# Optimization experiments

Hardware: AMD Instinct MI355X
Metric: run time of the kernel (lower is better)

Reference implementation:

```python
import jax, jax.numpy as jnp
import numpy as np

EPS = 1e-5  # InstanceNorm2d default eps


def setup_inputs() -> dict:
    key = jax.random.key(0)
    k1, k2, k3, k4, k5, k6 = jax.random.split(key, 6)
    B, N, C, KV, H = 8, 4096, 512, 960, 4
    dq, dk = C // 4, KV // 4
    emb1 = jax.random.normal(k1, (B, N, C), dtype=jnp.float32)
    emb_all = jax.random.normal(k2, (B, N, KV), dtype=jnp.float32)
    # per-head query Linear weights (torch Linear weight is [out, in]); 4 distinct heads
    Wq = jax.random.normal(k3, (H, dq, dq), dtype=jnp.float32) * 0.05
    # key/value: the original forward only ever uses key[0] / value[0]
    Wk = jax.random.normal(k4, (dk, dk), dtype=jnp.float32) * 0.05
    Wv = jax.random.normal(k5, (dk, dk), dtype=jnp.float32) * 0.05
    Wo = jax.random.normal(k6, (C, C), dtype=jnp.float32) * 0.05
    return {"emb1": emb1, "emb_all": emb_all, "Wq": Wq, "Wk": Wk, "Wv": Wv, "Wo": Wo}


def reference(emb1, emb_all, Wq, Wk, Wv, Wo):
    B, N, C = emb1.shape
    KV = emb_all.shape[2]
    dq, dk = C // 4, KV // 4
    # split emb1 into 4 chunks along channels -> [B, N, 4, dq], apply per-head query Linear
    Qc = emb1.reshape(B, N, 4, dq)
    Q = jnp.einsum("bnhd,hed->bhne", Qc, Wq)            # [B,4,N,dq]
    # all 4 K and V chunks use key[0]/value[0] (as in the source)
    Kc = emb_all.reshape(B, N, 4, dk)
    K = jnp.einsum("bnhd,ed->bhne", Kc, Wk)             # [B,4,N,dk]
    V = jnp.einsum("bnhd,ed->bhne", Kc, Wv)             # [B,4,N,dk]
    # channel attention: contract over tokens N -> scores [B,4,dq,dk]
    scores = jnp.einsum("bhnc,bhnk->bhck", Q, K) / jnp.sqrt(jnp.float32(KV))
    # InstanceNorm2d (no affine): normalize each (b, head) score map over (dq, dk)
    mu = scores.mean(axis=(2, 3), keepdims=True)
    var = scores.var(axis=(2, 3), keepdims=True)        # biased variance, matches torch
    normed = (scores - mu) * jax.lax.rsqrt(var + EPS)
    probs = jax.nn.softmax(normed, axis=3)              # softmax over dk
    # dropout is identity in eval mode
    context = jnp.einsum("bhck,bhnk->bhcn", probs, V)   # [B,4,dq,N]
    # permute(0,3,2,1) -> [B,N,dq,4], flatten last two -> [B,N,C]
    context = jnp.transpose(context, (0, 3, 2, 1)).reshape(B, N, C)
    O1 = jnp.einsum("bnc,ec->bne", context, Wo)         # out Linear, no bias
    return O1
```

## Files before the change

kernel.cpp:

```cpp
#include <hip/hip_runtime.h>
#include <cstdint>
#include <cstddef>

#define B_ 8
#define N_ 4096
#define C_ 512
#define KV_ 960
#define DQ 128
#define DK 240
#define NSPLIT 16

typedef __attribute__((ext_vector_type(8))) short bf16x8;
typedef __attribute__((ext_vector_type(4))) float f32x4;
#define AS1 __attribute__((address_space(1)))
#define AS3 __attribute__((address_space(3)))

__device__ __forceinline__ ushort f2bf(float f) {
  uint32_t u = __float_as_uint(f);
  u += 0x7FFFu + ((u >> 16) & 1u);
  return (ushort)(u >> 16);
}

__device__ __forceinline__ uint32_t cvtpk(float lo, float hi) {
  uint32_t r;
  asm("v_cvt_pk_bf16_f32 %0, %1, %2" : "=v"(r) : "v"(lo), "v"(hi));
  return r;
}

union bfpack {
  uint32_t u[4];
  ushort s[8];
  bf16x8 v;
};

__global__ __launch_bounds__(512) void k1_mfma(const float* __restrict__ emb1,
                                               const ushort* __restrict__ embaBF,
                                               float* __restrict__ P) {
  __shared__ ushort As[128 * 64];
  __shared__ ushort Bs[128 * 64];
  const int bh = blockIdx.x;
  const int split = blockIdx.y;
  const int jh = blockIdx.z;
  const int b = bh >> 2, h = bh & 3;
  const int t = threadIdx.x;
  const int w = t >> 6, l = t & 63;
  const int wm = w >> 1, wn = w & 1;

  const float* Abase = emb1 + (size_t)b * N_ * C_ + h * DQ;
  const ushort* Bbase = embaBF + (size_t)b * N_ * KV_;

  const int cA = t & 127;
  const int jB = t & 127;
  const int nb0 = t >> 7;
  int jl = jh * 128 + jB;
  if (jl > DK - 1) jl = DK - 1;
  const int jg = h * DK + jl;

  f32x4 acc[2][4];
#pragma unroll
  for (int fm = 0; fm < 2; ++fm)
#pragma unroll
    for (int fn = 0; fn < 4; ++fn) acc[fm][fn] = (f32x4){0.f, 0.f, 0.f, 0.f};

  const int n0 = split * (N_ / NSPLIT);
  const int lrow = l & 15;
  const int KS = (N_ / NSPLIT) / 64;

  float va[2][8];
  ushort ub[2][8];

#pragma unroll
  for (int q = 0; q < 2; ++q) {
    const float* g = Abase + (size_t)(n0 + (nb0 + q * 4) * 8) * C_ + cA;
#pragma unroll
    for (int kk = 0; kk < 8; ++kk) va[q][kk] = g[(size_t)kk * C_];
  }
#pragma unroll
  for (int q = 0; q < 2; ++q) {
    const ushort* g = Bbase + (size_t)(n0 + (nb0 + q * 4) * 8) * KV_ + jg;
#pragma unroll
    for (int kk = 0; kk < 8; ++kk) ub[q][kk] = g[(size_t)kk * KV_];
  }

  for (int ks = 0; ks < KS; ++ks) {
    bfpack pa[2], pb[2];
#pragma unroll
    for (int q = 0; q < 2; ++q)
#pragma unroll
      for (int p = 0; p < 4; ++p) pa[q].u[p] = cvtpk(va[q][2 * p], va[q][2 * p + 1]);
#pragma unroll
    for (int q = 0; q < 2; ++q)
#pragma unroll
      for (int kk = 0; kk < 8; ++kk) pb[q].s[kk] = ub[q][kk];

    __builtin_amdgcn_s_barrier();

#pragma unroll
    for (int q = 0; q < 2; ++q) {
      const int nb = nb0 + q * 4;
      *(bf16x8*)(As + cA * 64 + ((nb ^ (cA & 7)) << 3)) = pa[q].v;
      *(bf16x8*)(Bs + jB * 64 + ((nb ^ (jB & 7)) << 3)) = pb[q].v;
    }

    if (ks + 1 < KS) {
      const int nb1 = n0 + (ks + 1) * 64;
#pragma unroll
      for (int q = 0; q < 2; ++q) {
        const float* g = Abase + (size_t)(nb1 + (nb0 + q * 4) * 8) * C_ + cA;
#pragma unroll
        for (int kk = 0; kk < 8; ++kk) va[q][kk] = g[(size_t)kk * C_];
      }
#pragma unroll
      for (int q = 0; q < 2; ++q) {
        const ushort* g = Bbase + (size_t)(nb1 + (nb0 + q * 4) * 8) * KV_ + jg;
#pragma unroll
        for (int kk = 0; kk < 8; ++kk) ub[q][kk] = g[(size_t)kk * KV_];
      }
    }

    asm volatile("s_waitcnt lgkmcnt(0)" ::: "memory");
    __builtin_amdgcn_sched_barrier(0);
    __builtin_amdgcn_s_barrier();

#pragma unroll
    for (int half = 0; half < 2; ++half) {
      const int kb = half * 4 + (l >> 4);
      bf16x8 af[2], bv[4];
#pragma unroll
      for (int fm = 0; fm < 2; ++fm) {
        const int i = wm * 32 + fm * 16 + lrow;
        af[fm] = *(const bf16x8*)(As + i * 64 + ((kb ^ (i & 7)) << 3));
      }
#pragma unroll
      for (int fn = 0; fn < 4; ++fn) {
        const int j = wn * 64 + fn * 16 + lrow;
        bv[fn] = *(const bf16x8*)(Bs + j * 64 + ((kb ^ (j & 7)) << 3));
      }
#pragma unroll
      for (int fm = 0; fm < 2; ++fm)
#pragma unroll
        for (int fn = 0; fn < 4; ++fn)
          acc[fm][fn] = __builtin_amdgcn_mfma_f32_16x16x32_bf16(af[fm], bv[fn],
                                                                acc[fm][fn], 0, 0, 0);
    }
  }
  f32x4* Pv4 = (f32x4*)P + ((size_t)(split * 32 + bh) * 2 + jh) * 4096;
#pragma unroll
  for (int fm = 0; fm < 2; ++fm)
#pragma unroll
    for (int fn = 0; fn < 4; ++fn) Pv4[(fm * 4 + fn) * 512 + t] = acc[fm][fn];
}

__global__ __launch_bounds__(256) void k_reduce_frag(const f32x4* __restrict__ P,
                                                     float* __restrict__ S) {
  const int bh = blockIdx.x;
  const int g = blockIdx.y * 256 + threadIdx.x;
  const int jh = g >> 12;
  const int rest = g & 4095;
  f32x4 a = P[((size_t)bh * 2 + jh) * 4096 + rest];
#pragma unroll
  for (int s = 1; s < NSPLIT; ++s) {
    f32x4 v = P[((size_t)(s * 32 + bh) * 2 + jh) * 4096 + rest];
    a.x += v.x; a.y += v.y; a.z += v.z; a.w += v.w;
  }
  const int v = rest >> 9, tt = rest & 511;
  const int fm = v >> 2, fn = v & 3;
  const int wv = tt >> 6, l = tt & 63;
  const int wm = wv >> 1, wn = wv & 1;
  const int i0 = wm * 32 + fm * 16 + (l >> 4) * 4;
  const int j = jh * 128 + wn * 64 + fn * 16 + (l & 15);
  if (j < DK) {
    float* sp = S + (size_t)bh * (DQ * DK) + (size_t)i0 * DK + j;
    sp[0] = a.x; sp[DK] = a.y; sp[2 * DK] = a.z; sp[3 * DK] = a.w;
  }
}

__global__ __launch_bounds__(256) void k_cvt(const float4* __restrict__ in,
                                             ushort4* __restrict__ out, int n4) {
  int i = blockIdx.x * 256 + threadIdx.x;
  if (i >= n4) return;
  float4 v = in[i];
  ushort4 o;
  o.x = f2bf(v.x); o.y = f2bf(v.y); o.z = f2bf(v.z); o.w = f2bf(v.w);
  out[i] = o;
}

__global__ __launch_bounds__(256) void k_g1(const float* __restrict__ Wq,
                                            const float* __restrict__ S,
                                            float* __restrict__ U) {
  const int h = blockIdx.x, c0 = blockIdx.y * 64;
  const int b = blockIdx.z / 5, n0 = (blockIdx.z % 5) * 48;
  const float* A = Wq + (size_t)h * 16384;
  const float* Bp = S + (size_t)(b * 4 + h) * 30720 + n0;
  float* Cp = U + (size_t)(b * 4 + h) * 30720 + n0;
  __shared__ float Ast[16][65];
  __shared__ float Bst[16][49];
  const int t = threadIdx.x;
  const int mi = (t >> 4) * 4, nj = (t & 15) * 3;
  float acc[4][3] = {};
  for (int k0 = 0; k0 < 128; k0 += 16) {
    __syncthreads();
#pragma unroll
    for (int q = 0; q < 4; ++q) {
      int idx = t + q * 256, m = idx >> 4, k = idx & 15;
      Ast[k][m] = A[(size_t)(c0 + m) * 128 + k0 + k];
    }
#pragma unroll
    for (int q = 0; q < 3; ++q) {
      int idx = t + q * 256, k = idx / 48, n = idx % 48;
      Bst[k][n] = Bp[(size_t)(k0 + k) * 240 + n];
    }
    __syncthreads();
#pragma unroll
    for (int kk = 0; kk < 16; ++kk) {
      float a4[4], b3[3];
#pragma unroll
      for (int x = 0; x < 4; ++x) a4[x] = Ast[kk][mi + x];
#pragma unroll
      for (int y = 0; y < 3; ++y) b3[y] = Bst[kk][nj + y];
#pragma unroll
      for (int x = 0; x < 4; ++x)
#pragma unroll
        for (int y = 0; y < 3; ++y) acc[x][y] = fmaf(a4[x], b3[y], acc[x][y]);
    }
  }
#pragma unroll
  for (int x = 0; x < 4; ++x)
#pragma unroll
    for (int y = 0; y < 3; ++y)
      Cp[(size_t)(c0 + mi + x) * 240 + nj + y] = acc[x][y];
}

__global__ __launch_bounds__(256) void k_g2(const float* __restrict__ U,
                                            const float* __restrict__ Wk,
                                            float* __restrict__ SC) {
  const int m0 = blockIdx.x * 64, n0 = blockIdx.y * 48;
  __shared__ float Ast[16][65];
  __shared__ float Bst2[48][17];
  const int t = threadIdx.x;
  const int mi = (t >> 4) * 4, nj = (t & 15) * 3;
  float acc[4][3] = {};
  for (int k0 = 0; k0 < 240; k0 += 16) {
    __syncthreads();
#pragma unroll
    for (int q = 0; q < 4; ++q) {
      int idx = t + q * 256, m = idx >> 4, k = idx & 15;
      Ast[k][m] = U[(size_t)(m0 + m) * 240 + k0 + k];
    }
#pragma unroll
    for (int q = 0; q < 3; ++q) {
      int idx = t + q * 256, n = idx >> 4, kd = idx & 15;
      Bst2[n][kd] = Wk[(size_t)(n0 + n) * 240 + k0 + kd];
    }
    __syncthreads();
#pragma unroll
    for (int kk = 0; kk < 16; ++kk) {
      float a4[4], b3[3];
#pragma unroll
      for (int x = 0; x < 4; ++x) a4[x] = Ast[kk][mi + x];
#pragma unroll
      for (int y = 0; y < 3; ++y) b3[y] = Bst2[nj + y][kk];
#pragma unroll
      for (int x = 0; x < 4; ++x)
#pragma unroll
        for (int y = 0; y < 3; ++y) acc[x][y] = fmaf(a4[x], b3[y], acc[x][y]);
    }
  }
  const float scale = 0.0322748612183951f;
#pragma unroll
  for (int x = 0; x < 4; ++x)
#pragma unroll
    for (int y = 0; y < 3; ++y)
      SC[(size_t)(m0 + mi + x) * 240 + n0 + nj + y] = acc[x][y] * scale;
}

__global__ __launch_bounds__(256) void k_g3(const float* __restrict__ PR,
                                            const float* __restrict__ Wv,
                                            float* __restrict__ T) {
  const int m0 = blockIdx.x * 64, n0 = blockIdx.y * 48;
  __shared__ float Ast[16][65];
  __shared__ float Bst[16][49];
  const int t = threadIdx.x;
  const int mi = (t >> 4) * 4, nj = (t & 15) * 3;
  float acc[4][3] = {};
  for (int k0 = 0; k0 < 240; k0 += 16) {
    __syncthreads();
#pragma unroll
    for (int q = 0; q < 4; ++q) {
      int idx = t + q * 256, m = idx >> 4, k = idx & 15;
      Ast[k][m] = PR[(size_t)(m0 + m) * 240 + k0 + k];
    }
#pragma unroll
    for (int q = 0; q < 3; ++q) {
      int idx = t + q * 256, k = idx / 48, n = idx % 48;
      Bst[k][n] = Wv[(size_t)(k0 + k) * 240 + n0 + n];
    }
    __syncthreads();
#pragma unroll
    for (int kk = 0; kk < 16; ++kk) {
      float a4[4], b3[3];
#pragma unroll
      for (int x = 0; x < 4; ++x) a4[x] = Ast[kk][mi + x];
#pragma unroll
      for (int y = 0; y < 3; ++y) b3[y] = Bst[kk][nj + y];
#pragma unroll
      for (int x = 0; x < 4; ++x)
#pragma unroll
        for (int y = 0; y < 3; ++y) acc[x][y] = fmaf(a4[x], b3[y], acc[x][y]);
    }
  }
#pragma unroll
  for (int x = 0; x < 4; ++x)
#pragma unroll
    for (int y = 0; y < 3; ++y)
      T[(size_t)(m0 + mi + x) * 240 + n0 + nj + y] = acc[x][y];
}

__global__ __launch_bounds__(256) void k_g4(const float* __restrict__ Wo,
                                            const float* __restrict__ T,
                                            ushort* __restrict__ W3bf) {
  const int h = blockIdx.x, e0 = blockIdx.y * 64;
  const int b = blockIdx.z / 5, n0 = (blockIdx.z % 5) * 48;
  const float* Bp = T + (size_t)(b * 4 + h) * 30720 + n0;
  ushort* Cp = W3bf + (size_t)b * 491520 + h * 240 + n0;
  __shared__ float Ast[16][65];
  __shared__ float Bst[16][49];
  const int t = threadIdx.x;
  const int mi = (t >> 4) * 4, nj = (t & 15) * 3;
  float acc[4][3] = {};
  for (int k0 = 0; k0 < 128; k0 += 16) {
    __syncthreads();
#pragma unroll
    for (int q = 0; q < 4; ++q) {
      int idx = t + q * 256, m = idx >> 4, k = idx & 15;
      Ast[k][m] = Wo[(size_t)(e0 + m) * 512 + 4 * (k0 + k) + h];
    }
#pragma unroll
    for (int q = 0; q < 3; ++q) {
      int idx = t + q * 256, k = idx / 48, n = idx % 48;
      Bst[k][n] = Bp[(size_t)(k0 + k) * 240 + n];
    }
    __syncthreads();
#pragma unroll
    for (int kk = 0; kk < 16; ++kk) {
      float a4[4], b3[3];
#pragma unroll
      for (int x = 0; x < 4; ++x) a4[x] = Ast[kk][mi + x];
#pragma unroll
      for (int y = 0; y < 3; ++y) b3[y] = Bst[kk][nj + y];
#pragma unroll
      for (int x = 0; x < 4; ++x)
#pragma unroll
        for (int y = 0; y < 3; ++y) acc[x][y] = fmaf(a4[x], b3[y], acc[x][y]);
    }
  }
#pragma unroll
  for (int x = 0; x < 4; ++x)
#pragma unroll
    for (int y = 0; y < 3; ++y)
      Cp[(size_t)(e0 + mi + x) * 960 + nj + y] = f2bf(acc[x][y]);
}

__global__ __launch_bounds__(1024) void k_stats(const float* __restrict__ SC,
                                                float* __restrict__ stats) {
  const int bh = blockIdx.x;
  const float* s = SC + (size_t)bh * 30720;
  const int t = threadIdx.x;
  float sum = 0.f, sq = 0.f;
  for (int i = t; i < 30720; i += 1024) {
    float v = s[i];
    sum += v;
    sq = fmaf(v, v, sq);
  }
#pragma unroll
  for (int o = 32; o > 0; o >>= 1) {
    sum += __shfl_down(sum, o);
    sq += __shfl_down(sq, o);
  }
  __shared__ float s1[16], s2[16];
  if ((t & 63) == 0) { s1[t >> 6] = sum; s2[t >> 6] = sq; }
  __syncthreads();
  if (t == 0) {
    float ts = 0.f, tq = 0.f;
#pragma unroll
    for (int i = 0; i < 16; ++i) { ts += s1[i]; tq += s2[i]; }
    const float mu = ts * (1.f / 30720.f);
    const float var = tq * (1.f / 30720.f) - mu * mu;
    stats[bh * 2] = mu;
    stats[bh * 2 + 1] = rsqrtf(var + 1e-5f);
  }
}

__global__ __launch_bounds__(512) void k_softmax(const float* __restrict__ SC,
                                                 const float* __restrict__ stats,
                                                 float* __restrict__ PR) {
  const int bh = blockIdx.x;
  const float mu = stats[bh * 2], rstd = stats[bh * 2 + 1];
  const int wv = threadIdx.x >> 6, l = threadIdx.x & 63;
  const int row0 = blockIdx.y * 32 + wv * 4;
  const float* s = SC + (size_t)bh * 30720;
  float* p = PR + (size_t)bh * 30720;
#pragma unroll
  for (int r = 0; r < 4; ++r) {
    const float* srow = s + (size_t)(row0 + r) * 240;
    float* prow = p + (size_t)(row0 + r) * 240;
    float x0 = (srow[l] - mu) * rstd;
    float x1 = (srow[64 + l] - mu) * rstd;
    float x2 = (srow[128 + l] - mu) * rstd;
    float x3 = (l < 48) ? (srow[192 + l] - mu) * rstd : -1e30f;
    float m = fmaxf(fmaxf(x0, x1), fmaxf(x2, x3));
#pragma unroll
    for (int o = 32; o > 0; o >>= 1) m = fmaxf(m, __shfl_xor(m, o));
    float e0 = __expf(x0 - m), e1 = __expf(x1 - m), e2 = __expf(x2 - m);
    float e3 = (l < 48) ? __expf(x3 - m) : 0.f;
    float ss = e0 + e1 + e2 + e3;
#pragma unroll
    for (int o = 32; o > 0; o >>= 1) ss += __shfl_xor(ss, o);
    const float inv = 1.f / ss;
    prow[l] = e0 * inv;
    prow[64 + l] = e1 * inv;
    prow[128 + l] = e2 * inv;
    if (l < 48) prow[192 + l] = e3 * inv;
  }
}

__global__ __launch_bounds__(512) void k3_mfma(const ushort* __restrict__ A,
                                               const ushort* __restrict__ Bw,
                                               float* __restrict__ C) {
  __shared__ ushort LDSu[3][16384];
  const int bid = blockIdx.x;
  const int swz = (bid & 7) * 32 + (bid >> 3);
  const int b = swz >> 5;
  const int rem = swz & 31;
  const int mt = rem >> 1, nt = rem & 1;
  const int t = threadIdx.x;
  const int w = t >> 6, l = t & 63;
  const int wr = w >> 2, wc = w & 3;

  const ushort* Ab = A + (size_t)b * N_ * KV_ + (size_t)mt * 256 * KV_;
  const ushort* Bb = Bw + (size_t)b * C_ * KV_ + (size_t)nt * 256 * KV_;

  const int r_l = l & 15;
  const int c_l = (l >> 4) * 8;

#define K3STAGE(k0, bf)                                                        \
  do {                                                                         \
    _Pragma("unroll") for (int inst = 0; inst < 2; ++inst) {                   \
      const int g = w * 2 + inst;                             \
      const ushort* ga = Ab + (size_t)(g * 16 + r_l) * KV_ + (k0) + c_l;       \
      __builtin_amdgcn_global_load_lds(                                        \
          (AS1 const uint32_t*)(uintptr_t)ga,                                  \
          (AS3 uint32_t*)(uintptr_t)(&LDSu[bf][0] + g * 512), 16, 0, 0);       \
      const ushort* gb = Bb + (size_t)(g * 16 + r_l) * KV_ + (k0) + c_l;       \
      __builtin_amdgcn_global_load_lds(                                        \
          (AS1 const uint32_t*)(uintptr_t)gb,                                  \
          (AS3 uint32_t*)(uintptr_t)(&LDSu[bf][8192] + g * 512), 16, 0, 0);    \
    }                                                                          \
  } while (0)

  f32x4 acc[8][4];
#pragma unroll
  for (int fm = 0; fm < 8; ++fm)
#pragma unroll
    for (int fn = 0; fn < 4; ++fn) acc[fm][fn] = (f32x4){0.f, 0.f, 0.f, 0.f};

  K3STAGE(0, 0);
  K3STAGE(32, 1);

  const int NK = KV_ / 32;
  int cbuf = 0, sbuf = 2;
  for (int ks = 0; ks < NK; ++ks) {
    if (ks < NK - 1) asm volatile("s_waitcnt vmcnt(4)" ::: "memory");
    else             asm volatile("s_waitcnt vmcnt(0)" ::: "memory");
    __builtin_amdgcn_sched_barrier(0);
    __builtin_amdgcn_s_barrier();
    if (ks + 2 < NK) K3STAGE((ks + 2) * 32, sbuf);
    const ushort* Abase = &LDSu[cbuf][0];
    const ushort* Bbase = &LDSu[cbuf][8192];
    bf16x8 af[8], bv[4];
#pragma unroll
    for (int f = 0; f < 8; ++f)
      af[f] = *(const bf16x8*)(Abase + (wr * 8 + f) * 512 + l * 8);
#pragma unroll
    for (int f = 0; f < 4; ++f)
      bv[f] = *(const bf16x8*)(Bbase + (wc * 4 + f) * 512 + l * 8);
#pragma unroll
    for (int fm = 0; fm < 8; ++fm)
#pragma unroll
      for (int fn = 0; fn < 4; ++fn)
        acc[fm][fn] = __builtin_amdgcn_mfma_f32_16x16x32_bf16(af[fm], bv[fn],
                                                              acc[fm][fn], 0, 0, 0);
    cbuf = (cbuf == 2) ? 0 : cbuf + 1;
    sbuf = (sbuf == 2) ? 0 : sbuf + 1;
  }
#undef K3STAGE

  float* Cb = C + (size_t)b * N_ * C_ + ((size_t)mt * 256) * C_ + nt * 256;
  const int col = wc * 64 + (l & 15);
  const int rbase = wr * 128 + (l >> 4) * 4;
#pragma unroll
  for (int fm = 0; fm < 8; ++fm)
#pragma unroll
    for (int fn = 0; fn < 4; ++fn)
#pragma unroll
      for (int r = 0; r < 4; ++r)
        Cb[(size_t)(rbase + fm * 16 + r) * C_ + col + fn * 16] = acc[fm][fn][r];
}

extern "C" void kernel_launch(void* const* d_in, const int* in_sizes, int n_in,
                              void* d_out, int out_size, void* d_ws, size_t ws_size,
                              hipStream_t stream) {
  const float* emb1 = (const float*)d_in[0];
  const float* emba = (const float*)d_in[1];
  const float* Wq   = (const float*)d_in[2];
  const float* Wk   = (const float*)d_in[3];
  const float* Wv   = (const float*)d_in[4];
  const float* Wo   = (const float*)d_in[5];
  float* out = (float*)d_out;
  char* ws = (char*)d_ws;

  ushort* embaBF = (ushort*)(ws);
  float*  S      = (float*)(ws + 62914560);
  float*  T      = (float*)(ws + 62914560);
  float*  U      = (float*)(ws + 66846720);
  ushort* W3bf   = (ushort*)(ws + 66846720);
  float*  SCb    = (float*)(ws + 70778880);
  float*  PRb    = (float*)(ws + 74711040);
  float*  P      = out;
  float*  stats  = (float*)(ws + 66846720);

  k_cvt<<<30720, 256, 0, stream>>>((const float4*)emba, (ushort4*)embaBF, 7864320);

  k1_mfma<<<dim3(32, NSPLIT, 2), 512, 0, stream>>>(emb1, embaBF, P);
  k_reduce_frag<<<dim3(32, 32), 256, 0, stream>>>((const f32x4*)P, S);

  k_g1<<<dim3(4, 2, 40), 256, 0, stream>>>(Wq, S, U);
  k_g2<<<dim3(64, 5), 256, 0, stream>>>(U, Wk, SCb);
  k_stats<<<32, 1024, 0, stream>>>(SCb, stats);
  k_softmax<<<dim3(32, 4), 512, 0, stream>>>(SCb, stats, PRb);
  k_g3<<<dim3(64, 5), 256, 0, stream>>>(PRb, Wv, T);
  k_g4<<<dim3(4, 8, 40), 256, 0, stream>>>(Wo, T, W3bf);

  k3_mfma<<<256, 512, 0, stream>>>(embaBF, W3bf, out);
}
```

Before: 244.2 us.

## Fuse instance-norm stats with softmax; deepen k3 LDS pipeline and stage epilogue

Merges the stats and softmax kernels into one 1024-thread kernel that broadcasts mean and rstd through shared memory, removing a launch and a stats round-trip. The final bf16 MFMA GEMM moves from a 3-buffer to a 4-buffer LDS ring, prefetching three stages ahead with adjusted vmcnt waits. It also raises wave priority around the MFMA block and stages the output tile through LDS so the fp32 stores go out as coalesced float4 rows. The costs are more LDS per block (128KB), which may limit occupancy, and only 32 blocks for the fused softmax.

```diff
diff --git a/kernel.cpp b/kernel.cpp
--- a/kernel.cpp
+++ b/kernel.cpp
@@ -361,10 +361,11 @@
       Cp[(size_t)(e0 + mi + x) * 960 + nj + y] = f2bf(acc[x][y]);
 }
 
-__global__ __launch_bounds__(1024) void k_stats(const float* __restrict__ SC,
-                                                float* __restrict__ stats) {
+__global__ __launch_bounds__(1024) void k_inorm(const float* __restrict__ SC,
+                                                float* __restrict__ PR) {
   const int bh = blockIdx.x;
   const float* s = SC + (size_t)bh * 30720;
+  float* p = PR + (size_t)bh * 30720;
   const int t = threadIdx.x;
   float sum = 0.f, sq = 0.f;
   for (int i = t; i < 30720; i += 1024) {
@@ -377,7 +378,7 @@
     sum += __shfl_down(sum, o);
     sq += __shfl_down(sq, o);
   }
-  __shared__ float s1[16], s2[16];
+  __shared__ float s1[16], s2[16], bc[2];
   if ((t & 63) == 0) { s1[t >> 6] = sum; s2[t >> 6] = sq; }
   __syncthreads();
   if (t == 0) {
@@ -386,24 +387,17 @@
     for (int i = 0; i < 16; ++i) { ts += s1[i]; tq += s2[i]; }
     const float mu = ts * (1.f / 30720.f);
     const float var = tq * (1.f / 30720.f) - mu * mu;
-    stats[bh * 2] = mu;
-    stats[bh * 2 + 1] = rsqrtf(var + 1e-5f);
-  }
-}
-
-__global__ __launch_bounds__(512) void k_softmax(const float* __restrict__ SC,
-                                                 const float* __restrict__ stats,
-                                                 float* __restrict__ PR) {
-  const int bh = blockIdx.x;
-  const float mu = stats[bh * 2], rstd = stats[bh * 2 + 1];
-  const int wv = threadIdx.x >> 6, l = threadIdx.x & 63;
-  const int row0 = blockIdx.y * 32 + wv * 4;
-  const float* s = SC + (size_t)bh * 30720;
-  float* p = PR + (size_t)bh * 30720;
-#pragma unroll
-  for (int r = 0; r < 4; ++r) {
-    const float* srow = s + (size_t)(row0 + r) * 240;
-    float* prow = p + (size_t)(row0 + r) * 240;
+    bc[0] = mu;
+    bc[1] = rsqrtf(var + 1e-5f);
+  }
+  __syncthreads();
+  const float mu = bc[0], rstd = bc[1];
+  const int wv = t >> 6, l = t & 63;
+#pragma unroll
+  for (int r = 0; r < 8; ++r) {
+    const int row = wv * 8 + r;
+    const float* srow = s + (size_t)row * 240;
+    float* prow = p + (size_t)row * 240;
     float x0 = (srow[l] - mu) * rstd;
     float x1 = (srow[64 + l] - mu) * rstd;
     float x2 = (srow[128 + l] - mu) * rstd;
@@ -427,7 +421,7 @@
 __global__ __launch_bounds__(512) void k3_mfma(const ushort* __restrict__ A,
                                                const ushort* __restrict__ Bw,
                                                float* __restrict__ C) {
-  __shared__ ushort LDSu[3][16384];
+  __shared__ ushort LDSu[4][16384];
   const int bid = blockIdx.x;
   const int swz = (bid & 7) * 32 + (bid >> 3);
   const int b = swz >> 5;
@@ -466,15 +460,18 @@
 
   K3STAGE(0, 0);
   K3STAGE(32, 1);
+  K3STAGE(64, 2);
 
   const int NK = KV_ / 32;
-  int cbuf = 0, sbuf = 2;
   for (int ks = 0; ks < NK; ++ks) {
-    if (ks < NK - 1) asm volatile("s_waitcnt vmcnt(4)" ::: "memory");
-    else             asm volatile("s_waitcnt vmcnt(0)" ::: "memory");
+    const int nrem = NK - 1 - ks;
+    if (nrem >= 2)      asm volatile("s_waitcnt vmcnt(8)" ::: "memory");
+    else if (nrem == 1) asm volatile("s_waitcnt vmcnt(4)" ::: "memory");
+    else                asm volatile("s_waitcnt vmcnt(0)" ::: "memory");
     __builtin_amdgcn_sched_barrier(0);
     __builtin_amdgcn_s_barrier();
-    if (ks + 2 < NK) K3STAGE((ks + 2) * 32, sbuf);
+    if (ks + 3 < NK) K3STAGE((ks + 3) * 32, (ks + 3) & 3);
+    const int cbuf = ks & 3;
     const ushort* Abase = &LDSu[cbuf][0];
     const ushort* Bbase = &LDSu[cbuf][8192];
     bf16x8 af[8], bv[4];
@@ -484,27 +481,34 @@
 #pragma unroll
     for (int f = 0; f < 4; ++f)
       bv[f] = *(const bf16x8*)(Bbase + (wc * 4 + f) * 512 + l * 8);
+    __builtin_amdgcn_s_setprio(1);
 #pragma unroll
     for (int fm = 0; fm < 8; ++fm)
 #pragma unroll
       for (int fn = 0; fn < 4; ++fn)
         acc[fm][fn] = __builtin_amdgcn_mfma_f32_16x16x32_bf16(af[fm], bv[fn],
                                                               acc[fm][fn], 0, 0, 0);
-    cbuf = (cbuf == 2) ? 0 : cbuf + 1;
-    sbuf = (sbuf == 2) ? 0 : sbuf + 1;
+    __builtin_amdgcn_s_setprio(0);
   }
 #undef K3STAGE
 
-  float* Cb = C + (size_t)b * N_ * C_ + ((size_t)mt * 256) * C_ + nt * 256;
-  const int col = wc * 64 + (l & 15);
-  const int rbase = wr * 128 + (l >> 4) * 4;
-#pragma unroll
-  for (int fm = 0; fm < 8; ++fm)
+  __builtin_amdgcn_s_barrier();
+  float* lw = (float*)&LDSu[0][0] + (size_t)w * (16 * 68);
+  float* Cb = C + (size_t)b * N_ * C_ + ((size_t)mt * 256 + wr * 128) * C_ +
+              nt * 256 + wc * 64;
+#pragma unroll
+  for (int fm = 0; fm < 8; ++fm) {
 #pragma unroll
     for (int fn = 0; fn < 4; ++fn)
 #pragma unroll
       for (int r = 0; r < 4; ++r)
-        Cb[(size_t)(rbase + fm * 16 + r) * C_ + col + fn * 16] = acc[fm][fn][r];
+        lw[((l >> 4) * 4 + r) * 68 + (l & 15) + fn * 16] = acc[fm][fn][r];
+#pragma unroll
+    for (int q = 0; q < 4; ++q) {
+      float4 v = *(const float4*)(lw + (4 * q + (l >> 4)) * 68 + (l & 15) * 4);
+      *(float4*)(Cb + (size_t)(fm * 16 + 4 * q + (l >> 4)) * C_ + (l & 15) * 4) = v;
+    }
+  }
 }
 
 extern "C" void kernel_launch(void* const* d_in, const int* in_sizes, int n_in,
@@ -527,7 +531,6 @@
   float*  SCb    = (float*)(ws + 70778880);
   float*  PRb    = (float*)(ws + 74711040);
   float*  P      = out;
-  float*  stats  = (float*)(ws + 66846720);
 
   k_cvt<<<30720, 256, 0, stream>>>((const float4*)emba, (ushort4*)embaBF, 7864320);
 
@@ -536,8 +539,7 @@
 
   k_g1<<<dim3(4, 2, 40), 256, 0, stream>>>(Wq, S, U);
   k_g2<<<dim3(64, 5), 256, 0, stream>>>(U, Wk, SCb);
-  k_stats<<<32, 1024, 0, stream>>>(SCb, stats);
-  k_softmax<<<dim3(32, 4), 512, 0, stream>>>(SCb, stats, PRb);
+  k_inorm<<<32, 1024, 0, stream>>>(SCb, PRb);
   k_g3<<<dim3(64, 5), 256, 0, stream>>>(PRb, Wv, T);
   k_g4<<<dim3(4, 8, 40), 256, 0, stream>>>(Wo, T, W3bf);
 
```

New measurement: 246.6 us. Within noise of the previous version (+1.0%).

## Vectorize k1 global loads to pairs and fuse instance-norm stats with softmax

Applied to the files above, without the earlier changes.

The k1 staging loads now fetch two adjacent channels per thread (float2 for emb1, ushort2 for bf16 emb_all), and each thread writes two LDS rows with an adjusted XOR swizzle keyed on row>>1. This halves the number of scalar strided global loads and widens each access. Separately, the stats and softmax kernels are merged into one 1024-thread kernel per (b,h) that broadcasts mean and rstd through shared memory, removing a launch and the stats round trip at the cost of fewer blocks (32) doing the softmax.

```diff
diff --git a/kernel.cpp b/kernel.cpp
--- a/kernel.cpp
+++ b/kernel.cpp
@@ -49,12 +49,11 @@
   const float* Abase = emb1 + (size_t)b * N_ * C_ + h * DQ;
   const ushort* Bbase = embaBF + (size_t)b * N_ * KV_;
 
-  const int cA = t & 127;
-  const int jB = t & 127;
-  const int nb0 = t >> 7;
-  int jl = jh * 128 + jB;
-  if (jl > DK - 1) jl = DK - 1;
-  const int jg = h * DK + jl;
+  const int cp2 = (t & 63) * 2;
+  const int rg = t >> 6;
+  int jl0 = jh * 128 + cp2;
+  if (jl0 > 238) jl0 = 238;
+  const int jg0 = h * DK + jl0;
 
   f32x4 acc[2][4];
 #pragma unroll
@@ -65,57 +64,45 @@
   const int n0 = split * (N_ / NSPLIT);
   const int lrow = l & 15;
   const int KS = (N_ / NSPLIT) / 64;
-
-  float va[2][8];
-  ushort ub[2][8];
-
-#pragma unroll
-  for (int q = 0; q < 2; ++q) {
-    const float* g = Abase + (size_t)(n0 + (nb0 + q * 4) * 8) * C_ + cA;
-#pragma unroll
-    for (int kk = 0; kk < 8; ++kk) va[q][kk] = g[(size_t)kk * C_];
-  }
-#pragma unroll
-  for (int q = 0; q < 2; ++q) {
-    const ushort* g = Bbase + (size_t)(n0 + (nb0 + q * 4) * 8) * KV_ + jg;
-#pragma unroll
-    for (int kk = 0; kk < 8; ++kk) ub[q][kk] = g[(size_t)kk * KV_];
+  const int swA = (rg ^ ((cp2 >> 1) & 7)) << 3;
+
+  float2 va[8];
+  ushort2 ub[8];
+
+  {
+    const float* gA = Abase + (size_t)(n0 + rg * 8) * C_ + cp2;
+    const ushort* gB = Bbase + (size_t)(n0 + rg * 8) * KV_ + jg0;
+#pragma unroll
+    for (int kk = 0; kk < 8; ++kk) va[kk] = *(const float2*)(gA + (size_t)kk * C_);
+#pragma unroll
+    for (int kk = 0; kk < 8; ++kk) ub[kk] = *(const ushort2*)(gB + (size_t)kk * KV_);
   }
 
   for (int ks = 0; ks < KS; ++ks) {
-    bfpack pa[2], pb[2];
-#pragma unroll
-    for (int q = 0; q < 2; ++q)
-#pragma unroll
-      for (int p = 0; p < 4; ++p) pa[q].u[p] = cvtpk(va[q][2 * p], va[q][2 * p + 1]);
-#pragma unroll
-    for (int q = 0; q < 2; ++q)
-#pragma unroll
-      for (int kk = 0; kk < 8; ++kk) pb[q].s[kk] = ub[q][kk];
+    bfpack paL, paR, pbL, pbR;
+#pragma unroll
+    for (int p = 0; p < 4; ++p) {
+      paL.u[p] = cvtpk(va[2 * p].x, va[2 * p + 1].x);
+      paR.u[p] = cvtpk(va[2 * p].y, va[2 * p + 1].y);
+    }
+#pragma unroll
+    for (int kk = 0; kk < 8; ++kk) { pbL.s[kk] = ub[kk].x; pbR.s[kk] = ub[kk].y; }
 
     __builtin_amdgcn_s_barrier();
 
-#pragma unroll
-    for (int q = 0; q < 2; ++q) {
-      const int nb = nb0 + q * 4;
-      *(bf16x8*)(As + cA * 64 + ((nb ^ (cA & 7)) << 3)) = pa[q].v;
-      *(bf16x8*)(Bs + jB * 64 + ((nb ^ (jB & 7)) << 3)) = pb[q].v;
-    }
+    *(bf16x8*)(As + cp2 * 64 + swA) = paL.v;
+    *(bf16x8*)(As + (cp2 + 1) * 64 + swA) = paR.v;
+    *(bf16x8*)(Bs + cp2 * 64 + swA) = pbL.v;
+    *(bf16x8*)(Bs + (cp2 + 1) * 64 + swA) = pbR.v;
 
     if (ks + 1 < KS) {
       const int nb1 = n0 + (ks + 1) * 64;
-#pragma unroll
-      for (int q = 0; q < 2; ++q) {
-        const float* g = Abase + (size_t)(nb1 + (nb0 + q * 4) * 8) * C_ + cA;
-#pragma unroll
-        for (int kk = 0; kk < 8; ++kk) va[q][kk] = g[(size_t)kk * C_];
-      }
-#pragma unroll
-      for (int q = 0; q < 2; ++q) {
-        const ushort* g = Bbase + (size_t)(nb1 + (nb0 + q * 4) * 8) * KV_ + jg;
-#pragma unroll
-        for (int kk = 0; kk < 8; ++kk) ub[q][kk] = g[(size_t)kk * KV_];
-      }
+      const float* gA = Abase + (size_t)(nb1 + rg * 8) * C_ + cp2;
+      const ushort* gB = Bbase + (size_t)(nb1 + rg * 8) * KV_ + jg0;
+#pragma unroll
+      for (int kk = 0; kk < 8; ++kk) va[kk] = *(const float2*)(gA + (size_t)kk * C_);
+#pragma unroll
+      for (int kk = 0; kk < 8; ++kk) ub[kk] = *(const ushort2*)(gB + (size_t)kk * KV_);
     }
 
     asm volatile("s_waitcnt lgkmcnt(0)" ::: "memory");
@@ -129,12 +116,12 @@
 #pragma unroll
       for (int fm = 0; fm < 2; ++fm) {
         const int i = wm * 32 + fm * 16 + lrow;
-        af[fm] = *(const bf16x8*)(As + i * 64 + ((kb ^ (i & 7)) << 3));
+        af[fm] = *(const bf16x8*)(As + i * 64 + ((kb ^ ((i >> 1) & 7)) << 3));
       }
 #pragma unroll
       for (int fn = 0; fn < 4; ++fn) {
         const int j = wn * 64 + fn * 16 + lrow;
-        bv[fn] = *(const bf16x8*)(Bs + j * 64 + ((kb ^ (j & 7)) << 3));
+        bv[fn] = *(const bf16x8*)(Bs + j * 64 + ((kb ^ ((j >> 1) & 7)) << 3));
       }
 #pragma unroll
       for (int fm = 0; fm < 2; ++fm)
@@ -361,10 +348,11 @@
       Cp[(size_t)(e0 + mi + x) * 960 + nj + y] = f2bf(acc[x][y]);
 }
 
-__global__ __launch_bounds__(1024) void k_stats(const float* __restrict__ SC,
-                                                float* __restrict__ stats) {
+__global__ __launch_bounds__(1024) void k_inorm(const float* __restrict__ SC,
+                                                float* __restrict__ PR) {
   const int bh = blockIdx.x;
   const float* s = SC + (size_t)bh * 30720;
+  float* p = PR + (size_t)bh * 30720;
   const int t = threadIdx.x;
   float sum = 0.f, sq = 0.f;
   for (int i = t; i < 30720; i += 1024) {
@@ -377,7 +365,7 @@
     sum += __shfl_down(sum, o);
     sq += __shfl_down(sq, o);
   }
-  __shared__ float s1[16], s2[16];
+  __shared__ float s1[16], s2[16], bc[2];
   if ((t & 63) == 0) { s1[t >> 6] = sum; s2[t >> 6] = sq; }
   __syncthreads();
   if (t == 0) {
@@ -386,24 +374,17 @@
     for (int i = 0; i < 16; ++i) { ts += s1[i]; tq += s2[i]; }
     const float mu = ts * (1.f / 30720.f);
     const float var = tq * (1.f / 30720.f) - mu * mu;
-    stats[bh * 2] = mu;
-    stats[bh * 2 + 1] = rsqrtf(var + 1e-5f);
-  }
-}
-
-__global__ __launch_bounds__(512) void k_softmax(const float* __restrict__ SC,
-                                                 const float* __restrict__ stats,
-                                                 float* __restrict__ PR) {
-  const int bh = blockIdx.x;
-  const float mu = stats[bh * 2], rstd = stats[bh * 2 + 1];
-  const int wv = threadIdx.x >> 6, l = threadIdx.x & 63;
-  const int row0 = blockIdx.y * 32 + wv * 4;
-  const float* s = SC + (size_t)bh * 30720;
-  float* p = PR + (size_t)bh * 30720;
-#pragma unroll
-  for (int r = 0; r < 4; ++r) {
-    const float* srow = s + (size_t)(row0 + r) * 240;
-    float* prow = p + (size_t)(row0 + r) * 240;
+    bc[0] = mu;
+    bc[1] = rsqrtf(var + 1e-5f);
+  }
+  __syncthreads();
+  const float mu = bc[0], rstd = bc[1];
+  const int wv = t >> 6, l = t & 63;
+#pragma unroll
+  for (int r = 0; r < 8; ++r) {
+    const int row = wv * 8 + r;
+    const float* srow = s + (size_t)row * 240;
+    float* prow = p + (size_t)row * 240;
     float x0 = (srow[l] - mu) * rstd;
     float x1 = (srow[64 + l] - mu) * rstd;
     float x2 = (srow[128 + l] - mu) * rstd;
@@ -446,7 +427,7 @@
 #define K3STAGE(k0, bf)                                                        \
   do {                                                                         \
     _Pragma("unroll") for (int inst = 0; inst < 2; ++inst) {                   \
-      const int g = w * 2 + inst;                             \
+      const int g = w * 2 + inst;                                              \
       const ushort* ga = Ab + (size_t)(g * 16 + r_l) * KV_ + (k0) + c_l;       \
       __builtin_amdgcn_global_load_lds(                                        \
           (AS1 const uint32_t*)(uintptr_t)ga,                                  \
@@ -527,7 +508,6 @@
   float*  SCb    = (float*)(ws + 70778880);
   float*  PRb    = (float*)(ws + 74711040);
   float*  P      = out;
-  float*  stats  = (float*)(ws + 66846720);
 
   k_cvt<<<30720, 256, 0, stream>>>((const float4*)emba, (ushort4*)embaBF, 7864320);
 
@@ -536,8 +516,7 @@
 
   k_g1<<<dim3(4, 2, 40), 256, 0, stream>>>(Wq, S, U);
   k_g2<<<dim3(64, 5), 256, 0, stream>>>(U, Wk, SCb);
-  k_stats<<<32, 1024, 0, stream>>>(SCb, stats);
-  k_softmax<<<dim3(32, 4), 512, 0, stream>>>(SCb, stats, PRb);
+  k_inorm<<<32, 1024, 0, stream>>>(SCb, PRb);
   k_g3<<<dim3(64, 5), 256, 0, stream>>>(PRb, Wv, T);
   k_g4<<<dim3(4, 8, 40), 256, 0, stream>>>(Wo, T, W3bf);
 
```

New measurement: 243.4 us, median of 2. No clear change (-0.3%).
